# Performance work log

Measured on AMD Instinct MI355X. Metric: run time of the kernel, lower is better.

The kernel has to match this reference:

```python
import jax, jax.numpy as jnp
import numpy as np

UPDATE_STEPS = 2
EPS = 1e-7


def _collect(attn, source, W, b):
    """_Collection_Unit: relu(Linear(source)) gathered by attention, row-averaged.
    attn: [N_tgt, N_src], source: [N_src, D_in], W: [D_out, D_in], b: [D_out]."""
    fc_out = jax.nn.relu(source @ W.T + b)          # [N_src, D_out]
    collect = attn @ fc_out                          # [N_tgt, D_out]
    denom = jnp.sum(attn, axis=1, keepdims=True) + EPS
    return collect / denom


def setup_inputs() -> dict:
    key = jax.random.key(0)
    ks = jax.random.split(key, 10)
    N_OBJ, N_REL, D = 2048, 16384, 1024
    inp = {
        "obj_feats": jax.random.normal(ks[0], (N_OBJ, D), jnp.float32),
        "rel_feats": jax.random.normal(ks[1], (N_REL, D), jnp.float32),
        "attn_sub": jax.random.uniform(ks[2], (N_OBJ, N_REL), jnp.float32),
        "attn_obj": jax.random.uniform(ks[3], (N_OBJ, N_REL), jnp.float32),
        "attn_self": jax.random.uniform(ks[4], (N_OBJ, N_OBJ), jnp.float32),
    }
    # normal_init(fc, 0, 0.01) per original module
    names = ["rel2obj_sub", "rel2obj_obj", "obj2rel_sub", "obj2rel_obj", "obj2obj"]
    for i, n in enumerate(names):
        inp[f"W_{n}"] = jax.random.normal(ks[5 + i], (D, D), jnp.float32) * 0.01
        inp[f"b_{n}"] = jnp.zeros((D,), jnp.float32)
    return inp


def reference(obj_feats, rel_feats, attn_sub, attn_obj, attn_self,
              W_rel2obj_sub, b_rel2obj_sub, W_rel2obj_obj, b_rel2obj_obj,
              W_obj2rel_sub, b_obj2rel_sub, W_obj2rel_obj, b_obj2rel_obj,
              W_obj2obj, b_obj2obj):
    x_obj, x_rel = obj_feats, rel_feats
    for _ in range(UPDATE_STEPS):
        # collect to objects: from relations (as subject / as object) and from other objects
        src_sub = _collect(attn_sub, x_rel, W_rel2obj_sub, b_rel2obj_sub)   # unit 0
        src_obj = _collect(attn_obj, x_rel, W_rel2obj_obj, b_rel2obj_obj)   # unit 1
        src_self = _collect(attn_self, x_obj, W_obj2obj, b_obj2obj)         # unit 4
        src2obj = (src_sub + src_obj + src_self) / 3.0
        x_obj_new = x_obj + src2obj                                          # _Update_Unit 0
        # collect to relations: from subject / object node features
        src_rel_sub = _collect(attn_sub.T, x_obj, W_obj2rel_sub, b_obj2rel_sub)  # unit 2
        src_rel_obj = _collect(attn_obj.T, x_obj, W_obj2rel_obj, b_obj2rel_obj)  # unit 3
        src2rel = (src_rel_sub + src_rel_obj) / 2.0
        x_rel = x_rel + src2rel                                              # _Update_Unit 1
        x_obj = x_obj_new
    return x_obj, x_rel
```

## Files before the change

kernel.cpp:

```cpp
#include <hip/hip_runtime.h>
#include <hip/hip_bf16.h>

typedef __attribute__((ext_vector_type(4))) float  f32x4;
typedef __attribute__((ext_vector_type(8))) __bf16 bf16x8;
typedef __attribute__((ext_vector_type(4))) int    i32x4;
typedef __attribute__((ext_vector_type(8))) int    i32x8;
typedef __hip_bfloat16 bf16_t;

#define NOBJ 2048
#define NREL 16384
#define DIM  1024
#define KOBJ 34816
#define KREL 4096

#define AS1Q __attribute__((address_space(1)))
#define AS3Q __attribute__((address_space(3)))

__device__ __forceinline__ void gload_lds16(const void* g, void* l) {
    __builtin_amdgcn_global_load_lds((AS1Q void*)const_cast<void*>(g),
                                     (AS3Q void*)l, 16, 0, 0);
}

#define MFMA_F8(ACC, Af, Bf) \
    ACC = __builtin_amdgcn_mfma_scale_f32_16x16x128_f8f6f4( \
        Af, Bf, ACC, 0, 0, 0, 0x7F7F7F7F, 0, 0x7F7F7F7F)

__device__ __forceinline__ unsigned char fp8_byte(float x) {
    return (unsigned char)(__builtin_amdgcn_cvt_pk_fp8_f32(x, x, 0, false) & 0xFF);
}
__device__ __forceinline__ unsigned pk4_fp8(float a, float b, float c, float d) {
    int v = __builtin_amdgcn_cvt_pk_fp8_f32(a, b, 0, false);
    v = __builtin_amdgcn_cvt_pk_fp8_f32(c, d, v, true);
    return (unsigned)v;
}

__global__ __launch_bounds__(512, 4)
void gemmf8mlp(const unsigned char* __restrict__ W01, const unsigned char* __restrict__ xrel8,
               const unsigned char* __restrict__ W234, const unsigned char* __restrict__ xobj8,
               const float* __restrict__ b01, const float* __restrict__ bstk,
               unsigned char* __restrict__ fcObj8, unsigned char* __restrict__ fcRel8)
{
    __shared__ __align__(16) char lds[49152];

    const int tid  = threadIdx.x;
    const int lane = tid & 63;
    const int wid  = tid >> 6;
    const int wr = wid >> 2, wc = wid & 3;
    const int l15 = lane & 15, lk = lane >> 4;

    const int bid = blockIdx.x;
    const int s   = (bid & 7) * 152 + (bid >> 3);

    const unsigned char* A; const unsigned char* B; const float* bias; bool isFC;
    long rowM0, rowN0;
    if (s < 1024) {
        rowM0 = (long)(s >> 6) * 128;
        rowN0 = (long)(s & 63) * 256;
        A = W01; B = xrel8; bias = b01; isFC = true;
    } else {
        const int t = s - 1024;
        rowM0 = (long)(t >> 3) * 128;
        rowN0 = (long)(t & 7) * 256;
        A = W234; B = xobj8; bias = bstk; isFC = false;
    }
    const long ld = DIM;
    const int  NT = DIM >> 7;

    const int rs = tid >> 3;
    const int kc = (tid & 7) ^ (rs & 7);
    const char* gA = (const char*)A + (rowM0 + rs) * ld + kc * 16;
    const char* gB = (const char*)B + (rowN0 + rs) * ld + kc * 16;
    char* lA = (char*)lds + tid * 16;
    char* lB = (char*)lds + 16384 + tid * 16;

    const int xc0 = ((2 * lk + 0) ^ (l15 & 7)) * 16;
    const int xc1 = ((2 * lk + 1) ^ (l15 & 7)) * 16;
    const int baseA = (wr * 64 + l15) * 128;
    const int baseB = 16384 + (wc * 64 + l15) * 128;

#define LDF8(dst, off) { \
    i32x4 lo_ = *(const i32x4*)((const char*)lds + (off) + xc0); \
    i32x4 hi_ = *(const i32x4*)((const char*)lds + (off) + xc1); \
    dst = __builtin_shufflevector(lo_, hi_, 0, 1, 2, 3, 4, 5, 6, 7); }

    f32x4 acc[4][4];
    #pragma unroll
    for (int i = 0; i < 4; i++)
        #pragma unroll
        for (int j = 0; j < 4; j++) acc[i][j] = f32x4{0.f, 0.f, 0.f, 0.f};

    for (int t = 0; t < NT; ++t) {
        const long kByte = (long)t * 128;
        gload_lds16(gA + kByte, lA);
        gload_lds16(gA + kByte + 64 * ld, lA + 8192);
        #pragma unroll
        for (int i = 0; i < 4; i++)
            gload_lds16(gB + kByte + (long)i * 64 * ld, lB + i * 8192);
        __syncthreads();

        i32x8 a[4];
        #pragma unroll
        for (int kf = 0; kf < 4; kf++) LDF8(a[kf], baseA + kf * 2048);
        #pragma unroll
        for (int j = 0; j < 4; j++) {
            i32x8 b;
            LDF8(b, baseB + j * 2048);
            #pragma unroll
            for (int kf = 0; kf < 4; kf++) MFMA_F8(acc[kf][j], a[kf], b);
        }
        __syncthreads();
    }
#undef LDF8

    #pragma unroll
    for (int kf = 0; kf < 4; kf++) {
        const long m0 = rowM0 + wr * 64 + kf * 16 + lk * 4;
        #pragma unroll
        for (int r = 0; r < 4; r++) {
            const long m = m0 + r;
            const float bs = 64.f * bias[m];
            #pragma unroll
            for (int j = 0; j < 4; j++) {
                const long n = rowN0 + wc * 64 + j * 16 + l15;
                const float v = fmaxf(acc[kf][j][r] + bs, 0.f);
                const unsigned char o = fp8_byte(v);
                if (isFC) {
                    fcObj8[(m & 1023) * (long)KOBJ + (m >> 10) * 16384 + n] = o;
                } else {
                    if (m < 1024)       fcRel8[m * (long)KREL + n] = o;
                    else if (m < 2048)  fcRel8[(m - 1024) * (long)KREL + 2048 + n] = o;
                    else                fcObj8[(m - 2048) * (long)KOBJ + 32768 + n] = o;
                }
            }
        }
    }
}

__global__ __launch_bounds__(512, 4)
void gemmf8_dual(const unsigned char* __restrict__ Ao, const unsigned char* __restrict__ Bo,
                 float* __restrict__ Co,
                 const unsigned char* __restrict__ Ar, const unsigned char* __restrict__ Br,
                 float* __restrict__ Cr, unsigned char* __restrict__ xrel8out)
{
    __shared__ __align__(16) char lds[49152];

    const int tid  = threadIdx.x;
    const int lane = tid & 63;
    const int wid  = tid >> 6;
    const int wr = wid >> 2, wc = wid & 3;
    const int l15 = lane & 15, lk = lane >> 4;

    const int bid = blockIdx.x;
    const int s   = (bid & 7) * 128 + (bid >> 3);

    const unsigned char* A; const unsigned char* B; float* C;
    int K, NT; long kb0; float scale; bool at;
    long rowM0, rowN0;
    if (s < 512) {
        const int zz = s >> 6, t = s & 63;
        rowM0 = (long)(t >> 2) * 128; rowN0 = (long)(t & 3) * 256;
        A = Ao; B = Bo; C = Co;
        K = KOBJ; NT = 34; kb0 = (long)34 * zz * 128;
        scale = 1.f / (8192.f * 64.f); at = true;
    } else {
        const int t = s - 512;
        rowM0 = (long)(t >> 2) * 128; rowN0 = (long)(t & 3) * 256;
        A = Ar; B = Br; C = Cr;
        K = KREL; NT = 32; kb0 = 0;
        scale = 1.f / (2048.f * 64.f); at = false;
    }
    const long ld = (long)K;

    const int rs = tid >> 3;
    const int kc = (tid & 7) ^ (rs & 7);
    const char* gA = (const char*)A + (rowM0 + rs) * ld + kb0 + kc * 16;
    const char* gB = (const char*)B + (rowN0 + rs) * ld + kb0 + kc * 16;
    char* lA = (char*)lds + tid * 16;
    char* lB = (char*)lds + 16384 + tid * 16;

    const int xc0 = ((2 * lk + 0) ^ (l15 & 7)) * 16;
    const int xc1 = ((2 * lk + 1) ^ (l15 & 7)) * 16;
    const int baseA = (wr * 64 + l15) * 128;
    const int baseB = 16384 + (wc * 64 + l15) * 128;

#define LDF8(dst, off) { \
    i32x4 lo_ = *(const i32x4*)((const char*)lds + (off) + xc0); \
    i32x4 hi_ = *(const i32x4*)((const char*)lds + (off) + xc1); \
    dst = __builtin_shufflevector(lo_, hi_, 0, 1, 2, 3, 4, 5, 6, 7); }

    f32x4 acc[4][4];
    #pragma unroll
    for (int i = 0; i < 4; i++)
        #pragma unroll
        for (int j = 0; j < 4; j++) acc[i][j] = f32x4{0.f, 0.f, 0.f, 0.f};

    for (int t = 0; t < NT; ++t) {
        const long kByte = (long)t * 128;
        gload_lds16(gA + kByte, lA);
        gload_lds16(gA + kByte + 64 * ld, lA + 8192);
        #pragma unroll
        for (int i = 0; i < 4; i++)
            gload_lds16(gB + kByte + (long)i * 64 * ld, lB + i * 8192);
        __syncthreads();

        i32x8 a[4];
        #pragma unroll
        for (int kf = 0; kf < 4; kf++) LDF8(a[kf], baseA + kf * 2048);
        #pragma unroll
        for (int j = 0; j < 4; j++) {
            i32x8 b;
            LDF8(b, baseB + j * 2048);
            #pragma unroll
            for (int kf = 0; kf < 4; kf++) MFMA_F8(acc[kf][j], a[kf], b);
        }
        __syncthreads();
    }
#undef LDF8

    #pragma unroll
    for (int kf = 0; kf < 4; kf++) {
        const long m0 = rowM0 + wr * 64 + kf * 16 + lk * 4;
        #pragma unroll
        for (int r = 0; r < 4; r++) {
            const long m = m0 + r;
            #pragma unroll
            for (int j = 0; j < 4; j++) {
                const long n = rowN0 + wc * 64 + j * 16 + l15;
                const float v = acc[kf][j][r] * scale;
                const long idx = m * (long)DIM + n;
                if (at) {
                    atomicAdd(&C[idx], v);
                } else {
                    const float nv = C[idx] + v;
                    C[idx] = nv;
                    xrel8out[idx] = fp8_byte(nv);
                }
            }
        }
    }
}

__global__ __launch_bounds__(256)
void k_cast_fp8(const float* __restrict__ in, unsigned char* __restrict__ out,
                long n, float scale)
{
    const long stride = (long)gridDim.x * blockDim.x;
    for (long i = (long)blockIdx.x * blockDim.x + threadIdx.x; i * 4 < n; i += stride) {
        f32x4 v = *reinterpret_cast<const f32x4*>(in + i * 4);
        *reinterpret_cast<unsigned*>(out + i * 4) =
            pk4_fp8(v[0] * scale, v[1] * scale, v[2] * scale, v[3] * scale);
    }
}

template<bool COLS>
__global__ __launch_bounds__(256)
void k_sums(const float* __restrict__ in, int C,
            float* __restrict__ rowsum, float* __restrict__ colsum)
{
    __shared__ float cpart[16][64];
    __shared__ float rpart[64][17];
    const int tid = threadIdx.x;
    const int tx  = tid & 15;
    const int ty  = tid >> 4;
    const long c0 = (long)blockIdx.x * 64;
    const long r0 = (long)blockIdx.y * 64;

    float cs0 = 0.f, cs1 = 0.f, cs2 = 0.f, cs3 = 0.f;
    #pragma unroll
    for (int i = 0; i < 4; i++) {
        const int r = i * 16 + ty;
        const f32x4 v = *reinterpret_cast<const f32x4*>(&in[(r0 + r) * (long)C + c0 + tx * 4]);
        rpart[r][tx] = v[0] + v[1] + v[2] + v[3];
        cs0 += v[0]; cs1 += v[1]; cs2 += v[2]; cs3 += v[3];
    }
    if (COLS) {
        cpart[ty][tx * 4 + 0] = cs0;
        cpart[ty][tx * 4 + 1] = cs1;
        cpart[ty][tx * 4 + 2] = cs2;
        cpart[ty][tx * 4 + 3] = cs3;
    }
    __syncthreads();
    if (tid < 64) {
        float rs = 0.f;
        #pragma unroll
        for (int k = 0; k < 16; k++) rs += rpart[tid][k];
        atomicAdd(&rowsum[r0 + tid], rs);
        if (COLS) {
            float cs = 0.f;
            #pragma unroll
            for (int k = 0; k < 16; k++) cs += cpart[k][tid];
            atomicAdd(&colsum[c0 + tid], cs);
        }
    }
}

__global__ __launch_bounds__(256)
void k_invscale(float* __restrict__ s, int n, float c)
{
    const int i = blockIdx.x * 256 + threadIdx.x;
    if (i < n) s[i] = c / (s[i] + 1e-7f);
}

template<bool TRANS>
__global__ __launch_bounds__(256)
void k_prep2f8(const float* __restrict__ in, int C,
               unsigned char* __restrict__ Aobj, unsigned char* __restrict__ Arel,
               const float* __restrict__ invRow, const float* __restrict__ invCol)
{
    __shared__ float tile[64][65];
    const int tid = threadIdx.x;
    const int tx  = tid & 15;
    const int ty  = tid >> 4;
    const long c0 = (long)blockIdx.x * 64;
    const long r0 = (long)blockIdx.y * 64;

    #pragma unroll
    for (int i = 0; i < 4; i++) {
        const int r = i * 16 + ty;
        const f32x4 v = *reinterpret_cast<const f32x4*>(&in[(r0 + r) * (long)C + c0 + tx * 4]);
        const float sc = invRow[r0 + r];
        *reinterpret_cast<unsigned*>(&Aobj[(r0 + r) * (long)KOBJ + c0 + tx * 4]) =
            pk4_fp8(v[0] * sc, v[1] * sc, v[2] * sc, v[3] * sc);
        if (TRANS) *reinterpret_cast<f32x4*>(&tile[r][tx * 4]) = v;
    }
    if (TRANS) {
        __syncthreads();
        const int rr = tid & 63;
        const int cg = tid >> 6;
        #pragma unroll
        for (int i = 0; i < 16; i++) {
            const int c = cg * 16 + i;
            const float sc = invCol[c0 + c];
            Arel[(c0 + c) * (long)KREL + r0 + rr] = fp8_byte(tile[rr][c] * sc);
        }
    }
}

extern "C" void kernel_launch(void* const* d_in, const int* in_sizes, int n_in,
                              void* d_out, int out_size, void* d_ws, size_t ws_size,
                              hipStream_t stream)
{
    if (n_in < 15) return;
    const float* obj_feats = (const float*)d_in[0];
    const float* rel_feats = (const float*)d_in[1];
    const float* attn_sub  = (const float*)d_in[2];
    const float* attn_obj  = (const float*)d_in[3];
    const float* attn_self = (const float*)d_in[4];
    const float* Wf[5] = { (const float*)d_in[5], (const float*)d_in[7],
                           (const float*)d_in[9], (const float*)d_in[11], (const float*)d_in[13] };
    const float* Bf[5] = { (const float*)d_in[6], (const float*)d_in[8],
                           (const float*)d_in[10], (const float*)d_in[12], (const float*)d_in[14] };

    const int NO = NOBJ, NR = NREL, D = DIM;

    char* w = (char*)d_ws;
    auto take = [&](size_t bytes) { char* p = w; w += bytes; return p; };
    unsigned char* Aobj8  = (unsigned char*)take((size_t)NO * KOBJ);
    unsigned char* Arel8  = (unsigned char*)take((size_t)NR * KREL);
    unsigned char* fcObj8 = (unsigned char*)take((size_t)D * KOBJ);
    unsigned char* fcRel8 = (unsigned char*)take((size_t)D * KREL);
    unsigned char* xrel8  = (unsigned char*)take((size_t)NR * D);
    unsigned char* xobj8  = (unsigned char*)take((size_t)NO * D);
    unsigned char* W018   = (unsigned char*)take((size_t)2 * D * D);
    unsigned char* W2348  = (unsigned char*)take((size_t)3 * D * D);
    float*  b01     = (float*)take((size_t)2 * D * 4);
    float*  bstk    = (float*)take((size_t)3 * D * 4);
    float*  sums    = (float*)take((size_t)(3 * NO + 2 * NR) * 4);
    float* invS     = sums;
    float* invO     = sums + NO;
    float* invSelf  = sums + 2 * NO;
    float* invTS    = sums + 3 * NO;
    float* invTO    = sums + 3 * NO + NR;
    if ((size_t)(w - (char*)d_ws) > ws_size) return;

    float* x_obj = (float*)d_out;
    float* x_rel = x_obj + (size_t)NO * D;

    hipMemcpyAsync(x_obj, obj_feats, (size_t)NO * D * 4, hipMemcpyDeviceToDevice, stream);
    hipMemcpyAsync(x_rel, rel_feats, (size_t)NR * D * 4, hipMemcpyDeviceToDevice, stream);
    hipMemcpyAsync(b01,     Bf[0], (size_t)D * 4, hipMemcpyDeviceToDevice, stream);
    hipMemcpyAsync(b01 + D, Bf[1], (size_t)D * 4, hipMemcpyDeviceToDevice, stream);
    for (int i = 0; i < 3; i++)
        hipMemcpyAsync(bstk + i * D, Bf[2 + i], (size_t)D * 4, hipMemcpyDeviceToDevice, stream);
    hipMemsetAsync(sums, 0, (size_t)(3 * NO + 2 * NR) * 4, stream);

    auto cast8 = [&](const float* in, unsigned char* out, long n, float sc) {
        long blocks = (n / 4 + 255) / 256; if (blocks > 4096) blocks = 4096;
        k_cast_fp8<<<dim3((unsigned)blocks), dim3(256), 0, stream>>>(in, out, n, sc);
    };
    cast8(Wf[0], W018,                 (long)D * D, 64.f);
    cast8(Wf[1], W018 + (size_t)D * D, (long)D * D, 64.f);
    for (int i = 0; i < 3; i++)
        cast8(Wf[2 + i], W2348 + (size_t)i * D * D, (long)D * D, 64.f);

    k_sums<true><<<dim3(NR / 64, NO / 64), dim3(256), 0, stream>>>(attn_sub, NR, invS, invTS);
    k_sums<true><<<dim3(NR / 64, NO / 64), dim3(256), 0, stream>>>(attn_obj, NR, invO, invTO);
    k_sums<false><<<dim3(NO / 64, NO / 64), dim3(256), 0, stream>>>(attn_self, NO, invSelf, nullptr);
    k_invscale<<<dim3((3 * NO + 255) / 256), dim3(256), 0, stream>>>(sums, 3 * NO, 8192.f / 3.f);
    k_invscale<<<dim3((2 * NR + 255) / 256), dim3(256), 0, stream>>>(sums + 3 * NO, 2 * NR, 1024.f);

    k_prep2f8<true><<<dim3(NR / 64, NO / 64), dim3(256), 0, stream>>>(
        attn_sub, NR, Aobj8, Arel8, invS, invTS);
    k_prep2f8<true><<<dim3(NR / 64, NO / 64), dim3(256), 0, stream>>>(
        attn_obj, NR, Aobj8 + 16384, Arel8 + 2048, invO, invTO);
    k_prep2f8<false><<<dim3(NO / 64, NO / 64), dim3(256), 0, stream>>>(
        attn_self, NO, Aobj8 + 32768, nullptr, invSelf, nullptr);

    cast8(x_rel, xrel8, (long)NR * D, 1.f);

    for (int step = 0; step < 2; ++step) {
        cast8(x_obj, xobj8, (long)NO * D, 1.f);

        gemmf8mlp<<<dim3(1216), dim3(512), 0, stream>>>(
            W018, xrel8, W2348, xobj8, b01, bstk, fcObj8, fcRel8);

        gemmf8_dual<<<dim3(1024), dim3(512), 0, stream>>>(
            Aobj8, fcObj8, x_obj, Arel8, fcRel8, x_rel, xrel8);
    }
}
```

Before: 772.0 us.

## Fuse attention row/col sums into fp8 prep pass, apply normalisation in GEMM accumulators

The attention matrices were previously read twice, once to compute row and column sums and again to quantise with per-row normalisation. Now a single pass quantises them to fp8 with a fixed scale while accumulating the sums. The per-segment normalisation is moved into the dual GEMM: accumulators are rescaled by ratios at segment boundaries and by a final per-row factor in the epilogue. This saves a full read of the large attention tensors, at the cost of extra multiplies inside the GEMM loop and a possible change in fp8 quantisation accuracy, since unnormalised values are scaled by a constant 16.

```diff
diff --git a/kernel.cpp b/kernel.cpp
--- a/kernel.cpp
+++ b/kernel.cpp
@@ -2,16 +2,15 @@
 #include <hip/hip_bf16.h>
 
 typedef __attribute__((ext_vector_type(4))) float  f32x4;
-typedef __attribute__((ext_vector_type(8))) __bf16 bf16x8;
 typedef __attribute__((ext_vector_type(4))) int    i32x4;
 typedef __attribute__((ext_vector_type(8))) int    i32x8;
-typedef __hip_bfloat16 bf16_t;
 
 #define NOBJ 2048
 #define NREL 16384
 #define DIM  1024
 #define KOBJ 34816
 #define KREL 4096
+#define EPS  1e-7f
 
 #define AS1Q __attribute__((address_space(1)))
 #define AS3Q __attribute__((address_space(3)))
@@ -140,7 +139,10 @@
 void gemmf8_dual(const unsigned char* __restrict__ Ao, const unsigned char* __restrict__ Bo,
                  float* __restrict__ Co,
                  const unsigned char* __restrict__ Ar, const unsigned char* __restrict__ Br,
-                 float* __restrict__ Cr, unsigned char* __restrict__ xrel8out)
+                 float* __restrict__ Cr, unsigned char* __restrict__ xrel8out,
+                 const float* __restrict__ rat1, const float* __restrict__ rat2,
+                 const float* __restrict__ finO,
+                 const float* __restrict__ ratR, const float* __restrict__ finR)
 {
     __shared__ __align__(16) char lds[49152];
 
@@ -154,22 +156,25 @@
     const int s   = (bid & 7) * 128 + (bid >> 3);
 
     const unsigned char* A; const unsigned char* B; float* C;
-    int K, NT; long kb0; float scale; bool at;
+    const float* finP;
+    int K, NT; long kb0; bool isObj;
     long rowM0, rowN0;
     if (s < 512) {
         const int zz = s >> 6, t = s & 63;
         rowM0 = (long)(t >> 2) * 128; rowN0 = (long)(t & 3) * 256;
-        A = Ao; B = Bo; C = Co;
+        A = Ao; B = Bo; C = Co; finP = finO;
         K = KOBJ; NT = 34; kb0 = (long)34 * zz * 128;
-        scale = 1.f / (8192.f * 64.f); at = true;
+        isObj = true;
     } else {
         const int t = s - 512;
         rowM0 = (long)(t >> 2) * 128; rowN0 = (long)(t & 3) * 256;
-        A = Ar; B = Br; C = Cr;
+        A = Ar; B = Br; C = Cr; finP = finR;
         K = KREL; NT = 32; kb0 = 0;
-        scale = 1.f / (2048.f * 64.f); at = false;
+        isObj = false;
     }
     const long ld = (long)K;
+    const int g0 = (int)(kb0 >> 7);
+    const int g1 = g0 + NT;
 
     const int rs = tid >> 3;
     const int kc = (tid & 7) ^ (rs & 7);
@@ -188,6 +193,16 @@
     i32x4 hi_ = *(const i32x4*)((const char*)lds + (off) + xc1); \
     dst = __builtin_shufflevector(lo_, hi_, 0, 1, 2, 3, 4, 5, 6, 7); }
 
+#define APPLY_RATIO(RP) { \
+    _Pragma("unroll") \
+    for (int kf = 0; kf < 4; kf++) { \
+        const f32x4 rv = *(const f32x4*)((RP) + rowM0 + wr * 64 + kf * 16 + lk * 4); \
+        _Pragma("unroll") \
+        for (int j = 0; j < 4; j++) \
+            _Pragma("unroll") \
+            for (int r = 0; r < 4; r++) acc[kf][j][r] *= rv[r]; \
+    } }
+
     f32x4 acc[4][4];
     #pragma unroll
     for (int i = 0; i < 4; i++)
@@ -213,22 +228,36 @@
             #pragma unroll
             for (int kf = 0; kf < 4; kf++) MFMA_F8(acc[kf][j], a[kf], b);
         }
+
+        if (isObj) {
+            const int g = g0 + t;
+            if (g + 1 == 128 && g1 > 128) APPLY_RATIO(rat1);
+            if (g + 1 == 256 && g1 > 256) APPLY_RATIO(rat2);
+        } else {
+            if (t + 1 == 16) APPLY_RATIO(ratR);
+        }
         __syncthreads();
     }
+    if (isObj) {
+        if (g0 < 128 && g1 <= 128) APPLY_RATIO(rat1);
+        if (g0 < 256 && g1 <= 256) APPLY_RATIO(rat2);
+    }
 #undef LDF8
+#undef APPLY_RATIO
 
     #pragma unroll
     for (int kf = 0; kf < 4; kf++) {
         const long m0 = rowM0 + wr * 64 + kf * 16 + lk * 4;
+        const f32x4 fv = *(const f32x4*)(finP + m0);
         #pragma unroll
         for (int r = 0; r < 4; r++) {
             const long m = m0 + r;
             #pragma unroll
             for (int j = 0; j < 4; j++) {
                 const long n = rowN0 + wc * 64 + j * 16 + l15;
-                const float v = acc[kf][j][r] * scale;
+                const float v = acc[kf][j][r] * fv[r];
                 const long idx = m * (long)DIM + n;
-                if (at) {
+                if (isObj) {
                     atomicAdd(&C[idx], v);
                 } else {
                     const float nv = C[idx] + v;
@@ -252,11 +281,13 @@
     }
 }
 
-template<bool COLS>
+template<bool TRANS>
 __global__ __launch_bounds__(256)
-void k_sums(const float* __restrict__ in, int C,
-            float* __restrict__ rowsum, float* __restrict__ colsum)
-{
+void k_prep16(const float* __restrict__ in, int C,
+              unsigned char* __restrict__ Aobj, unsigned char* __restrict__ Arel,
+              float* __restrict__ rowsum, float* __restrict__ colsum)
+{
+    __shared__ float tile[64][65];
     __shared__ float cpart[16][64];
     __shared__ float rpart[64][17];
     const int tid = threadIdx.x;
@@ -270,10 +301,13 @@
     for (int i = 0; i < 4; i++) {
         const int r = i * 16 + ty;
         const f32x4 v = *reinterpret_cast<const f32x4*>(&in[(r0 + r) * (long)C + c0 + tx * 4]);
+        *reinterpret_cast<unsigned*>(&Aobj[(r0 + r) * (long)KOBJ + c0 + tx * 4]) =
+            pk4_fp8(v[0] * 16.f, v[1] * 16.f, v[2] * 16.f, v[3] * 16.f);
         rpart[r][tx] = v[0] + v[1] + v[2] + v[3];
         cs0 += v[0]; cs1 += v[1]; cs2 += v[2]; cs3 += v[3];
-    }
-    if (COLS) {
+        if (TRANS) *reinterpret_cast<f32x4*>(&tile[r][tx * 4]) = v;
+    }
+    if (TRANS) {
         cpart[ty][tx * 4 + 0] = cs0;
         cpart[ty][tx * 4 + 1] = cs1;
         cpart[ty][tx * 4 + 2] = cs2;
@@ -281,59 +315,41 @@
     }
     __syncthreads();
     if (tid < 64) {
-        float rs = 0.f;
-        #pragma unroll
-        for (int k = 0; k < 16; k++) rs += rpart[tid][k];
-        atomicAdd(&rowsum[r0 + tid], rs);
-        if (COLS) {
-            float cs = 0.f;
+        float rsum = 0.f;
+        #pragma unroll
+        for (int k = 0; k < 16; k++) rsum += rpart[tid][k];
+        atomicAdd(&rowsum[r0 + tid], rsum);
+        if (TRANS) {
+            float csum = 0.f;
             #pragma unroll
-            for (int k = 0; k < 16; k++) cs += cpart[k][tid];
-            atomicAdd(&colsum[c0 + tid], cs);
-        }
-    }
-}
-
-__global__ __launch_bounds__(256)
-void k_invscale(float* __restrict__ s, int n, float c)
-{
-    const int i = blockIdx.x * 256 + threadIdx.x;
-    if (i < n) s[i] = c / (s[i] + 1e-7f);
-}
-
-template<bool TRANS>
-__global__ __launch_bounds__(256)
-void k_prep2f8(const float* __restrict__ in, int C,
-               unsigned char* __restrict__ Aobj, unsigned char* __restrict__ Arel,
-               const float* __restrict__ invRow, const float* __restrict__ invCol)
-{
-    __shared__ float tile[64][65];
-    const int tid = threadIdx.x;
-    const int tx  = tid & 15;
-    const int ty  = tid >> 4;
-    const long c0 = (long)blockIdx.x * 64;
-    const long r0 = (long)blockIdx.y * 64;
-
-    #pragma unroll
-    for (int i = 0; i < 4; i++) {
-        const int r = i * 16 + ty;
-        const f32x4 v = *reinterpret_cast<const f32x4*>(&in[(r0 + r) * (long)C + c0 + tx * 4]);
-        const float sc = invRow[r0 + r];
-        *reinterpret_cast<unsigned*>(&Aobj[(r0 + r) * (long)KOBJ + c0 + tx * 4]) =
-            pk4_fp8(v[0] * sc, v[1] * sc, v[2] * sc, v[3] * sc);
-        if (TRANS) *reinterpret_cast<f32x4*>(&tile[r][tx * 4]) = v;
+            for (int k = 0; k < 16; k++) csum += cpart[k][tid];
+            atomicAdd(&colsum[c0 + tid], csum);
+        }
     }
     if (TRANS) {
-        __syncthreads();
         const int rr = tid & 63;
         const int cg = tid >> 6;
         #pragma unroll
         for (int i = 0; i < 16; i++) {
             const int c = cg * 16 + i;
-            const float sc = invCol[c0 + c];
-            Arel[(c0 + c) * (long)KREL + r0 + rr] = fp8_byte(tile[rr][c] * sc);
-        }
-    }
+            Arel[(c0 + c) * (long)KREL + r0 + rr] = fp8_byte(tile[rr][c] * 16.f);
+        }
+    }
+}
+
+__global__ __launch_bounds__(256)
+void k_mkscales(const float* __restrict__ r1, const float* __restrict__ r2,
+                const float* __restrict__ r3,
+                float* __restrict__ rat1, float* __restrict__ rat2,
+                float* __restrict__ fin, int n, float finDiv)
+{
+    const int i = blockIdx.x * 256 + threadIdx.x;
+    if (i >= n) return;
+    const float a = r1[i] + EPS, b = r2[i] + EPS;
+    const float c = r3 ? (r3[i] + EPS) : b;
+    rat1[i] = b / a;
+    if (rat2) rat2[i] = c / b;
+    fin[i] = 1.f / (c * finDiv);
 }
 
 extern "C" void kernel_launch(void* const* d_in, const int* in_sizes, int n_in,
@@ -366,11 +382,17 @@
     float*  b01     = (float*)take((size_t)2 * D * 4);
     float*  bstk    = (float*)take((size_t)3 * D * 4);
     float*  sums    = (float*)take((size_t)(3 * NO + 2 * NR) * 4);
-    float* invS     = sums;
-    float* invO     = sums + NO;
-    float* invSelf  = sums + 2 * NO;
-    float* invTS    = sums + 3 * NO;
-    float* invTO    = sums + 3 * NO + NR;
+    float*  scl     = (float*)take((size_t)(3 * NO + 2 * NR) * 4);
+    float* rsumS  = sums;
+    float* rsumO  = sums + NO;
+    float* rsumSf = sums + 2 * NO;
+    float* csumS  = sums + 3 * NO;
+    float* csumO  = sums + 3 * NO + NR;
+    float* rat1 = scl;
+    float* rat2 = scl + NO;
+    float* finO = scl + 2 * NO;
+    float* ratR = scl + 3 * NO;
+    float* finR = scl + 3 * NO + NR;
     if ((size_t)(w - (char*)d_ws) > ws_size) return;
 
     float* x_obj = (float*)d_out;
@@ -393,18 +415,17 @@
     for (int i = 0; i < 3; i++)
         cast8(Wf[2 + i], W2348 + (size_t)i * D * D, (long)D * D, 64.f);
 
-    k_sums<true><<<dim3(NR / 64, NO / 64), dim3(256), 0, stream>>>(attn_sub, NR, invS, invTS);
-    k_sums<true><<<dim3(NR / 64, NO / 64), dim3(256), 0, stream>>>(attn_obj, NR, invO, invTO);
-    k_sums<false><<<dim3(NO / 64, NO / 64), dim3(256), 0, stream>>>(attn_self, NO, invSelf, nullptr);
-    k_invscale<<<dim3((3 * NO + 255) / 256), dim3(256), 0, stream>>>(sums, 3 * NO, 8192.f / 3.f);
-    k_invscale<<<dim3((2 * NR + 255) / 256), dim3(256), 0, stream>>>(sums + 3 * NO, 2 * NR, 1024.f);
-
-    k_prep2f8<true><<<dim3(NR / 64, NO / 64), dim3(256), 0, stream>>>(
-        attn_sub, NR, Aobj8, Arel8, invS, invTS);
-    k_prep2f8<true><<<dim3(NR / 64, NO / 64), dim3(256), 0, stream>>>(
-        attn_obj, NR, Aobj8 + 16384, Arel8 + 2048, invO, invTO);
-    k_prep2f8<false><<<dim3(NO / 64, NO / 64), dim3(256), 0, stream>>>(
-        attn_self, NO, Aobj8 + 32768, nullptr, invSelf, nullptr);
+    k_prep16<true><<<dim3(NR / 64, NO / 64), dim3(256), 0, stream>>>(
+        attn_sub, NR, Aobj8, Arel8, rsumS, csumS);
+    k_prep16<true><<<dim3(NR / 64, NO / 64), dim3(256), 0, stream>>>(
+        attn_obj, NR, Aobj8 + 16384, Arel8 + 2048, rsumO, csumO);
+    k_prep16<false><<<dim3(NO / 64, NO / 64), dim3(256), 0, stream>>>(
+        attn_self, NO, Aobj8 + 32768, nullptr, rsumSf, nullptr);
+
+    k_mkscales<<<dim3((NO + 255) / 256), dim3(256), 0, stream>>>(
+        rsumS, rsumO, rsumSf, rat1, rat2, finO, NO, 3072.f);
+    k_mkscales<<<dim3((NR + 255) / 256), dim3(256), 0, stream>>>(
+        csumS, csumO, nullptr, ratR, nullptr, finR, NR, 2048.f);
 
     cast8(x_rel, xrel8, (long)NR * D, 1.f);
 
@@ -415,6 +436,7 @@
             W018, xrel8, W2348, xobj8, b01, bstk, fcObj8, fcRel8);
 
         gemmf8_dual<<<dim3(1024), dim3(512), 0, stream>>>(
-            Aobj8, fcObj8, x_obj, Arel8, fcRel8, x_rel, xrel8);
-    }
-}
+            Aobj8, fcObj8, x_obj, Arel8, fcRel8, x_rel, xrel8,
+            rat1, rat2, finO, ratR, finR);
+    }
+}
```

Measured after the change: 1.448 ms. 87.5% more time.
